# Kernel tuning notes

Hardware: AMD Instinct MI355X
Metric: run time of the kernel (lower is better)

The kernel has to match this reference:

```python
import jax, jax.numpy as jnp
import numpy as np

N_VOX = 100000   # active voxels
K = 27           # 3^3 kernel offsets
M = 60000        # matched (in, out) pairs per offset
CIN = 64
COUT = 64
BN_EPS = 1e-5


def setup_inputs() -> dict:
    key = jax.random.key(0)
    ks = jax.random.split(key, 6)
    feats = jax.random.normal(ks[0], (N_VOX, CIN), dtype=jnp.float32)
    W = jax.random.normal(ks[1], (K, CIN, COUT), dtype=jnp.float32) * 0.05
    gamma = jnp.ones((COUT,), dtype=jnp.float32)
    beta = jnp.zeros((COUT,), dtype=jnp.float32)
    running_mean = jax.random.normal(ks[2], (COUT,), dtype=jnp.float32) * 0.1
    running_var = jax.random.uniform(ks[3], (COUT,), dtype=jnp.float32, minval=0.5, maxval=1.5)
    in_idx = jax.random.randint(ks[4], (K, M), 0, N_VOX, dtype=jnp.int32)
    out_idx = jax.random.randint(ks[5], (K, M), 0, N_VOX, dtype=jnp.int32)
    return {
        "feats": feats, "W": W, "gamma": gamma, "beta": beta,
        "running_mean": running_mean, "running_var": running_var,
        "in_idx": in_idx, "out_idx": out_idx,
    }


def reference(feats, W, gamma, beta, running_mean, running_var, in_idx, out_idx):
    # Sparse conv as gather-GEMM-scatter over the hash-map kernel map.
    gathered = feats[in_idx]                              # [K, M, Cin]
    contrib = jnp.einsum('kmc,kcd->kmd', gathered, W)     # [K, M, Cout]
    out = jax.ops.segment_sum(
        contrib.reshape(-1, W.shape[-1]),                 # [K*M, Cout]
        out_idx.reshape(-1),
        num_segments=feats.shape[0],
    )                                                     # [N, Cout]
    # BatchNorm (inference, running stats) + ReLU
    inv = jax.lax.rsqrt(running_var + BN_EPS)
    y = (out - running_mean) * (inv * gamma) + beta
    return jnp.maximum(y, 0.0)
```

## Files before the change

### kernel.cpp

```cpp
#include <hip/hip_runtime.h>

#define N_VOX 100000
#define K_OFF 27
#define M_PAIR 60000
#define NPAIR (K_OFF * M_PAIR)
#define CIN 64
#define COUT 64
#define BN_EPS 1e-5f

#define VB_SHIFT 8
#define VB (1 << VB_SHIFT)
#define NB ((N_VOX + VB - 1) / VB)
#define BCAP 5120
#define PPT 16
#define PA_PAIRS (256 * PPT)
#define PA_GRID ((NPAIR + PA_PAIRS - 1) / PA_PAIRS)

#define TILES_PER_WAVE 10
#define WAVES_PER_K (M_PAIR / 16 / TILES_PER_WAVE)
#define CONV_BLOCKS_X ((WAVES_PER_K + 3) / 4)

typedef __attribute__((ext_vector_type(8))) short bf16x8;
typedef __attribute__((ext_vector_type(8))) unsigned short u16x8;
typedef __attribute__((ext_vector_type(4))) unsigned int u32x4;
typedef __attribute__((ext_vector_type(2))) int i32x2;
typedef __attribute__((ext_vector_type(4))) float f32x4;

__device__ __forceinline__ unsigned short f32_to_bf16(float f) {
    unsigned int u = __float_as_uint(f);
    u += 0x7FFFu + ((u >> 16) & 1u);
    return (unsigned short)(u >> 16);
}
__device__ __forceinline__ float bf16_lo(unsigned int u) {
    return __uint_as_float(u << 16);
}
__device__ __forceinline__ float bf16_hi(unsigned int u) {
    return __uint_as_float(u & 0xffff0000u);
}

__global__ __launch_bounds__(256) void prep_kernel(
    const float* __restrict__ feats, unsigned short* __restrict__ fb,
    const float* __restrict__ W, unsigned short* __restrict__ Wt,
    const float* __restrict__ gamma, const float* __restrict__ beta,
    const float* __restrict__ rmean, const float* __restrict__ rvar,
    float* __restrict__ bnscale, float* __restrict__ bnshift,
    int* __restrict__ bucketCount)
{
    const int gid = blockIdx.x * 256 + threadIdx.x;
    const int nt = gridDim.x * 256;
    for (int e4i = gid; e4i < (N_VOX * CIN) / 4; e4i += nt) {
        const int e4 = e4i * 4;
        const float4 v = *(const float4*)(feats + e4);
        ushort4 b;
        b.x = f32_to_bf16(v.x);
        b.y = f32_to_bf16(v.y);
        b.z = f32_to_bf16(v.z);
        b.w = f32_to_bf16(v.w);
        *(ushort4*)(fb + e4) = b;
    }
    for (int e = gid; e < K_OFF * CIN * COUT; e += nt) {
        const int k = e / (CIN * COUT);
        const int r = e % (CIN * COUT);
        Wt[k * CIN * COUT + (r % COUT) * CIN + (r / COUT)] = f32_to_bf16(W[e]);
    }
    if (gid < COUT) {
        const float inv = rsqrtf(rvar[gid] + BN_EPS);
        const float sc = inv * gamma[gid];
        bnscale[gid] = sc;
        bnshift[gid] = beta[gid] - rmean[gid] * sc;
    }
    if (gid < NB) bucketCount[gid] = 0;
}

__global__ __launch_bounds__(256) void conv_bucket_kernel(
    const unsigned short* __restrict__ fb, const unsigned short* __restrict__ Wt,
    const int* __restrict__ in_idx, const int* __restrict__ oix,
    unsigned int* __restrict__ recs, int* __restrict__ bucketCount,
    unsigned short* __restrict__ contrib)
{
    __shared__ alignas(16) unsigned short lds[4][16 * 72];
    __shared__ int lhist[NB];
    __shared__ int gbase[NB];
    const int t = threadIdx.x;
    const int k = blockIdx.y;
    const int fid = k * CONV_BLOCKS_X + blockIdx.x;

    if (fid < PA_GRID) {
        for (int i = t; i < NB; i += 256) lhist[i] = 0;
        __syncthreads();
        const int base = fid * PA_PAIRS;
        int lp[PPT];
#pragma unroll
        for (int i = 0; i < PPT; ++i) {
            const int e = base + i * 256 + t;
            lp[i] = (e < NPAIR) ? atomicAdd(&lhist[oix[e] >> VB_SHIFT], 1) : 0;
        }
        __syncthreads();
        for (int i = t; i < NB; i += 256) {
            const int c = lhist[i];
            gbase[i] = c ? atomicAdd(&bucketCount[i], c) : 0;
        }
        __syncthreads();
#pragma unroll
        for (int i = 0; i < PPT; ++i) {
            const int e = base + i * 256 + t;
            if (e < NPAIR) {
                const int v = oix[e];
                const int b = v >> VB_SHIFT;
                const int idx = gbase[b] + lp[i];
                if (idx < BCAP)
                    recs[(size_t)b * BCAP + idx] =
                        ((unsigned int)e << VB_SHIFT) | (unsigned int)(v & (VB - 1));
            }
        }
    }

    const int lane = threadIdx.x & 63;
    const int wid = threadIdx.x >> 6;
    const int w = blockIdx.x * 4 + wid;
    if (w >= WAVES_PER_K) return;
    const int col = lane & 15;
    const int quad = lane >> 4;
    unsigned short* L = lds[wid];

    bf16x8 Bf[4][2];
    const short* Wk = (const short*)(Wt + k * CIN * COUT);
#pragma unroll
    for (int tt = 0; tt < 4; ++tt) {
        const short* p = Wk + (tt * 16 + col) * CIN + quad * 8;
        Bf[tt][0] = *(const bf16x8*)(p);
        Bf[tt][1] = *(const bf16x8*)(p + 32);
    }

    int m0 = k * M_PAIR + (w * TILES_PER_WAVE) * 16;
    {
        const int rin = in_idx[m0 + col];
        const short* fp = (const short*)fb + (size_t)rin * CIN + quad * 8;
        bf16x8 A0 = *(const bf16x8*)(fp);
        bf16x8 A1 = *(const bf16x8*)(fp + 32);

        for (int it = 0; it < TILES_PER_WAVE; ++it) {
            bf16x8 nA0 = A0, nA1 = A1;
            if (it + 1 < TILES_PER_WAVE) {
                const int rn = in_idx[m0 + 16 + col];
                const short* fn = (const short*)fb + (size_t)rn * CIN + quad * 8;
                nA0 = *(const bf16x8*)(fn);
                nA1 = *(const bf16x8*)(fn + 32);
            }

            f32x4 acc[4];
#pragma unroll
            for (int tt = 0; tt < 4; ++tt) {
                f32x4 z = {0.f, 0.f, 0.f, 0.f};
                acc[tt] = __builtin_amdgcn_mfma_f32_16x16x32_bf16(A0, Bf[tt][0], z, 0, 0, 0);
                acc[tt] = __builtin_amdgcn_mfma_f32_16x16x32_bf16(A1, Bf[tt][1], acc[tt], 0, 0, 0);
            }
#pragma unroll
            for (int r = 0; r < 4; ++r) {
                const int row = quad * 4 + r;
#pragma unroll
                for (int tt = 0; tt < 4; ++tt)
                    L[row * 72 + tt * 16 + col] = f32_to_bf16(acc[tt][r]);
            }
#pragma unroll
            for (int itr = 0; itr < 2; ++itr) {
                const int row = itr * 8 + (lane >> 3);
                const int chunk = lane & 7;
                const u16x8 v = *(const u16x8*)(L + row * 72 + chunk * 8);
                *(u16x8*)(contrib + (size_t)(m0 + row) * 64 + chunk * 8) = v;
            }
            A0 = nA0;
            A1 = nA1;
            m0 += 16;
        }
    }
}

__global__ __launch_bounds__(512) void perm_seg_kernel(
    const unsigned int* __restrict__ recs, const int* __restrict__ bucketCount,
    int* __restrict__ perm, i32x2* __restrict__ segcnt)
{
    __shared__ int scan[512];
    __shared__ int hist[VB];
    __shared__ int gb_sh, bc_sh;
    const int b = blockIdx.x;
    const int t = threadIdx.x;
    int c = 0;
    if (t < NB) {
        c = bucketCount[t];
        if (c > BCAP) c = BCAP;
    }
    scan[t] = c;
    __syncthreads();
    for (int o = 1; o < 512; o <<= 1) {
        int x = (t >= o) ? scan[t - o] : 0;
        __syncthreads();
        scan[t] += x;
        __syncthreads();
    }
    if (t == b) {
        gb_sh = scan[t] - c;
        bc_sh = c;
    }
    if (t < VB) hist[t] = 0;
    __syncthreads();
    const int bc = bc_sh;
    const int gbase = gb_sh;
    const unsigned int* r = recs + (size_t)b * BCAP;
    for (int i = t; i < bc; i += 512)
        atomicAdd(&hist[r[i] & (VB - 1)], 1);
    __syncthreads();
    int hc = 0;
    if (t < VB) {
        hc = hist[t];
        scan[t] = hc;
    }
    __syncthreads();
    for (int o = 1; o < VB; o <<= 1) {
        int x = (t < VB && t >= o) ? scan[t - o] : 0;
        __syncthreads();
        if (t < VB) scan[t] += x;
        __syncthreads();
    }
    if (t < VB) {
        const int excl = scan[t] - hc;
        const int v = b * VB + t;
        if (v < N_VOX) {
            i32x2 sc2;
            sc2.x = gbase + excl;
            sc2.y = hc;
            segcnt[v] = sc2;
        }
        hist[t] = excl;
    }
    __syncthreads();
    for (int i = t; i < bc; i += 512) {
        const unsigned int rec = r[i];
        const int lp = atomicAdd(&hist[rec & (VB - 1)], 1);
        perm[gbase + lp] = (int)(rec >> VB_SHIFT);
    }
}

__global__ __launch_bounds__(256) void gather_bn_kernel(
    const unsigned short* __restrict__ contrib, const int* __restrict__ perm,
    const i32x2* __restrict__ segcnt,
    const float* __restrict__ bnscale, const float* __restrict__ bnshift,
    float* __restrict__ out)
{
    const int v = blockIdx.x * 4 + (threadIdx.x >> 6);
    if (v >= N_VOX) return;
    const int lane = threadIdx.x & 63;
    const int rg = lane >> 3;
    const int cg = lane & 7;
    const i32x2 sc = segcnt[v];
    const int s = sc.x;
    const int n = sc.y;

    float a0 = 0.f, a1 = 0.f, a2 = 0.f, a3 = 0.f;
    float a4 = 0.f, a5 = 0.f, a6 = 0.f, a7 = 0.f;
    float b0 = 0.f, b1 = 0.f, b2 = 0.f, b3 = 0.f;
    float b4 = 0.f, b5 = 0.f, b6 = 0.f, b7 = 0.f;
    int j = rg;
    for (; j + 8 < n; j += 16) {
        const int p0 = perm[s + j];
        const int p1 = perm[s + j + 8];
        const u32x4 u = __builtin_nontemporal_load(
            (const u32x4*)(contrib + (size_t)p0 * 64) + cg);
        const u32x4 w = __builtin_nontemporal_load(
            (const u32x4*)(contrib + (size_t)p1 * 64) + cg);
        a0 += bf16_lo(u.x); a1 += bf16_hi(u.x);
        a2 += bf16_lo(u.y); a3 += bf16_hi(u.y);
        a4 += bf16_lo(u.z); a5 += bf16_hi(u.z);
        a6 += bf16_lo(u.w); a7 += bf16_hi(u.w);
        b0 += bf16_lo(w.x); b1 += bf16_hi(w.x);
        b2 += bf16_lo(w.y); b3 += bf16_hi(w.y);
        b4 += bf16_lo(w.z); b5 += bf16_hi(w.z);
        b6 += bf16_lo(w.w); b7 += bf16_hi(w.w);
    }
    for (; j < n; j += 8) {
        const int p0 = perm[s + j];
        const u32x4 u = __builtin_nontemporal_load(
            (const u32x4*)(contrib + (size_t)p0 * 64) + cg);
        a0 += bf16_lo(u.x); a1 += bf16_hi(u.x);
        a2 += bf16_lo(u.y); a3 += bf16_hi(u.y);
        a4 += bf16_lo(u.z); a5 += bf16_hi(u.z);
        a6 += bf16_lo(u.w); a7 += bf16_hi(u.w);
    }
    a0 += b0; a1 += b1; a2 += b2; a3 += b3;
    a4 += b4; a5 += b5; a6 += b6; a7 += b7;
    a0 += __shfl_xor(a0, 8, 64); a0 += __shfl_xor(a0, 16, 64); a0 += __shfl_xor(a0, 32, 64);
    a1 += __shfl_xor(a1, 8, 64); a1 += __shfl_xor(a1, 16, 64); a1 += __shfl_xor(a1, 32, 64);
    a2 += __shfl_xor(a2, 8, 64); a2 += __shfl_xor(a2, 16, 64); a2 += __shfl_xor(a2, 32, 64);
    a3 += __shfl_xor(a3, 8, 64); a3 += __shfl_xor(a3, 16, 64); a3 += __shfl_xor(a3, 32, 64);
    a4 += __shfl_xor(a4, 8, 64); a4 += __shfl_xor(a4, 16, 64); a4 += __shfl_xor(a4, 32, 64);
    a5 += __shfl_xor(a5, 8, 64); a5 += __shfl_xor(a5, 16, 64); a5 += __shfl_xor(a5, 32, 64);
    a6 += __shfl_xor(a6, 8, 64); a6 += __shfl_xor(a6, 16, 64); a6 += __shfl_xor(a6, 32, 64);
    a7 += __shfl_xor(a7, 8, 64); a7 += __shfl_xor(a7, 16, 64); a7 += __shfl_xor(a7, 32, 64);
    if (rg == 0) {
        const int ch = cg * 8;
        float4 r0, r1;
        r0.x = fmaxf(fmaf(a0, bnscale[ch + 0], bnshift[ch + 0]), 0.f);
        r0.y = fmaxf(fmaf(a1, bnscale[ch + 1], bnshift[ch + 1]), 0.f);
        r0.z = fmaxf(fmaf(a2, bnscale[ch + 2], bnshift[ch + 2]), 0.f);
        r0.w = fmaxf(fmaf(a3, bnscale[ch + 3], bnshift[ch + 3]), 0.f);
        r1.x = fmaxf(fmaf(a4, bnscale[ch + 4], bnshift[ch + 4]), 0.f);
        r1.y = fmaxf(fmaf(a5, bnscale[ch + 5], bnshift[ch + 5]), 0.f);
        r1.z = fmaxf(fmaf(a6, bnscale[ch + 6], bnshift[ch + 6]), 0.f);
        r1.w = fmaxf(fmaf(a7, bnscale[ch + 7], bnshift[ch + 7]), 0.f);
        *(float4*)(out + (size_t)v * 64 + ch) = r0;
        *(float4*)(out + (size_t)v * 64 + ch + 4) = r1;
    }
}

__global__ __launch_bounds__(256) void prep_small_kernel(
    const float* __restrict__ feats, unsigned short* __restrict__ fb,
    float* __restrict__ out, const float* __restrict__ W,
    unsigned short* __restrict__ Wt)
{
    const int e = blockIdx.x * blockDim.x + threadIdx.x;
    if (e < (N_VOX * CIN) / 4) {
        const int e4 = e * 4;
        const float4 v = *(const float4*)(feats + e4);
        ushort4 b;
        b.x = f32_to_bf16(v.x);
        b.y = f32_to_bf16(v.y);
        b.z = f32_to_bf16(v.z);
        b.w = f32_to_bf16(v.w);
        *(ushort4*)(fb + e4) = b;
        *(float4*)(out + e4) = make_float4(0.f, 0.f, 0.f, 0.f);
    }
    if (e < K_OFF * CIN * COUT) {
        const int k = e / (CIN * COUT);
        const int r = e % (CIN * COUT);
        Wt[k * CIN * COUT + (r % COUT) * CIN + (r / COUT)] = f32_to_bf16(W[e]);
    }
}

__global__ __launch_bounds__(256) void conv_atomic_kernel(
    const unsigned short* __restrict__ fb, const unsigned short* __restrict__ Wt,
    const int* __restrict__ in_idx, const int* __restrict__ out_idx,
    float* __restrict__ out)
{
    const int k = blockIdx.y;
    const int lane = threadIdx.x & 63;
    const int wave = blockIdx.x * 4 + (threadIdx.x >> 6);
    const int col = lane & 15;
    const int quad = lane >> 4;
    bf16x8 Bf[4][2];
    const short* Wk = (const short*)(Wt + k * CIN * COUT);
#pragma unroll
    for (int t = 0; t < 4; ++t) {
        const short* p = Wk + (t * 16 + col) * CIN + quad * 8;
        Bf[t][0] = *(const bf16x8*)(p);
        Bf[t][1] = *(const bf16x8*)(p + 32);
    }
    const int base = k * M_PAIR;
    for (int tile = wave; tile < M_PAIR / 16; tile += 128) {
        const int m0 = base + tile * 16;
        const int rin = in_idx[m0 + col];
        const short* fp = (const short*)fb + (size_t)rin * CIN + quad * 8;
        const bf16x8 A0 = *(const bf16x8*)(fp);
        const bf16x8 A1 = *(const bf16x8*)(fp + 32);
        f32x4 acc[4];
#pragma unroll
        for (int t = 0; t < 4; ++t) {
            f32x4 z = {0.f, 0.f, 0.f, 0.f};
            acc[t] = __builtin_amdgcn_mfma_f32_16x16x32_bf16(A0, Bf[t][0], z, 0, 0, 0);
            acc[t] = __builtin_amdgcn_mfma_f32_16x16x32_bf16(A1, Bf[t][1], acc[t], 0, 0, 0);
        }
        int vo[4];
#pragma unroll
        for (int r = 0; r < 4; ++r) vo[r] = out_idx[m0 + quad * 4 + r];
#pragma unroll
        for (int r = 0; r < 4; ++r) {
            float* op = out + (size_t)vo[r] * COUT + col;
#pragma unroll
            for (int t = 0; t < 4; ++t) atomicAdd(op + t * 16, acc[t][r]);
        }
    }
}

__global__ __launch_bounds__(256) void bn_relu_kernel(
    float* __restrict__ out,
    const float* __restrict__ gamma, const float* __restrict__ beta,
    const float* __restrict__ mean, const float* __restrict__ var)
{
    const int e = blockIdx.x * blockDim.x + threadIdx.x;
    if (e >= N_VOX * COUT) return;
    const int c = e & (COUT - 1);
    const float inv = rsqrtf(var[c] + BN_EPS);
    const float y = (out[e] - mean[c]) * (inv * gamma[c]) + beta[c];
    out[e] = fmaxf(y, 0.f);
}

extern "C" void kernel_launch(void* const* d_in, const int* in_sizes, int n_in,
                              void* d_out, int out_size, void* d_ws, size_t ws_size,
                              hipStream_t stream) {
    const float* feats = (const float*)d_in[0];
    const float* W     = (const float*)d_in[1];
    const float* gamma = (const float*)d_in[2];
    const float* beta  = (const float*)d_in[3];
    const float* rmean = (const float*)d_in[4];
    const float* rvar  = (const float*)d_in[5];
    const int* in_idx  = (const int*)d_in[6];
    const int* out_idx = (const int*)d_in[7];
    float* out = (float*)d_out;

    char* ws = (char*)d_ws;
    size_t off = 0;
    auto alloc = [&](size_t bytes) {
        size_t p = off;
        off = (off + bytes + 255) & ~(size_t)255;
        return p;
    };
    const size_t o_fb   = alloc((size_t)N_VOX * CIN * 2);
    const size_t o_wt   = alloc((size_t)K_OFF * CIN * COUT * 2);
    const size_t o_bc   = alloc((size_t)NB * 4);
    const size_t o_recs = alloc((size_t)NB * BCAP * 4);
    const size_t o_sc   = alloc((size_t)N_VOX * 8);
    const size_t o_bn   = alloc((size_t)2 * COUT * 4);
    const size_t o_perm = alloc((size_t)NPAIR * 4);
    const size_t o_ctr  = alloc((size_t)NPAIR * COUT * 2);
    const bool big = (ws_size >= off);

    unsigned short* fb  = (unsigned short*)(ws + o_fb);
    unsigned short* Wt  = (unsigned short*)(ws + o_wt);
    int* bucketCount    = (int*)(ws + o_bc);
    unsigned int* recs  = (unsigned int*)(ws + o_recs);
    i32x2* segcnt       = (i32x2*)(ws + o_sc);
    float* bnscale      = (float*)(ws + o_bn);
    float* bnshift      = bnscale + COUT;
    int* perm           = (int*)(ws + o_perm);
    unsigned short* ctr = (unsigned short*)(ws + o_ctr);

    if (big) {
        prep_kernel<<<2048, 256, 0, stream>>>(
            feats, fb, W, Wt, gamma, beta, rmean, rvar,
            bnscale, bnshift, bucketCount);
        conv_bucket_kernel<<<dim3(CONV_BLOCKS_X, K_OFF), 256, 0, stream>>>(
            fb, Wt, in_idx, out_idx, recs, bucketCount, ctr);
        perm_seg_kernel<<<NB, 512, 0, stream>>>(recs, bucketCount, perm, segcnt);
        gather_bn_kernel<<<(N_VOX + 3) / 4, 256, 0, stream>>>(
            ctr, perm, segcnt, bnscale, bnshift, out);
    } else {
        const int ptot = (N_VOX * CIN) / 4;
        prep_small_kernel<<<(ptot + 255) / 256, 256, 0, stream>>>(feats, fb, out, W, Wt);
        conv_atomic_kernel<<<dim3(32, K_OFF), 256, 0, stream>>>(fb, Wt, in_idx, out_idx, out);
        const int total_e = N_VOX * COUT;
        bn_relu_kernel<<<(total_e + 255) / 256, 256, 0, stream>>>(out, gamma, beta, rmean, rvar);
    }
}
```

Before: 228.0 us.

## Fuse per-bucket permutation build into gather+BN kernel using shared-memory local perm

Merges the per-bucket counting-sort kernel and the gather/BN/ReLU kernel. Each block now takes a quarter of a voxel bucket, builds its segment offsets and pair permutation in shared memory, then gathers the bf16 contributions and applies BN+ReLU. This drops the global perm and segcnt arrays and one launch. In exchange every block rescans the whole bucket's records, four times redundantly across the quarters, and uses only NB*4 blocks. A quarter holding more than QCAP pairs would be truncated.

```diff
diff --git a/kernel.cpp b/kernel.cpp
--- a/kernel.cpp
+++ b/kernel.cpp
@@ -16,6 +16,10 @@
 #define PA_PAIRS (256 * PPT)
 #define PA_GRID ((NPAIR + PA_PAIRS - 1) / PA_PAIRS)
 
+#define QSPLIT 4
+#define QVOX (VB / QSPLIT)
+#define QCAP 1280
+
 #define TILES_PER_WAVE 10
 #define WAVES_PER_K (M_PAIR / 16 / TILES_PER_WAVE)
 #define CONV_BLOCKS_X ((WAVES_PER_K + 3) / 4)
@@ -23,7 +27,6 @@
 typedef __attribute__((ext_vector_type(8))) short bf16x8;
 typedef __attribute__((ext_vector_type(8))) unsigned short u16x8;
 typedef __attribute__((ext_vector_type(4))) unsigned int u32x4;
-typedef __attribute__((ext_vector_type(2))) int i32x2;
 typedef __attribute__((ext_vector_type(4))) float f32x4;
 
 __device__ __forceinline__ unsigned short f32_to_bf16(float f) {
@@ -176,139 +179,117 @@
     }
 }
 
-__global__ __launch_bounds__(512) void perm_seg_kernel(
+__global__ __launch_bounds__(256) void gather_bn_kernel(
     const unsigned int* __restrict__ recs, const int* __restrict__ bucketCount,
-    int* __restrict__ perm, i32x2* __restrict__ segcnt)
-{
-    __shared__ int scan[512];
-    __shared__ int hist[VB];
-    __shared__ int gb_sh, bc_sh;
-    const int b = blockIdx.x;
+    const unsigned short* __restrict__ contrib,
+    const float* __restrict__ bnscale, const float* __restrict__ bnshift,
+    float* __restrict__ out)
+{
+    __shared__ int hist[QVOX];
+    __shared__ int scan_[QVOX];
+    __shared__ int cursor[QVOX];
+    __shared__ int lperm[QCAP];
+    __shared__ float s_sc[COUT], s_sh[COUT];
+    const int blk = blockIdx.x;
+    const int b = blk >> 2;
+    const int q = blk & 3;
     const int t = threadIdx.x;
-    int c = 0;
-    if (t < NB) {
-        c = bucketCount[t];
-        if (c > BCAP) c = BCAP;
-    }
-    scan[t] = c;
+    if (t < QVOX) hist[t] = 0;
+    if (t < COUT) { s_sc[t] = bnscale[t]; s_sh[t] = bnshift[t]; }
     __syncthreads();
-    for (int o = 1; o < 512; o <<= 1) {
-        int x = (t >= o) ? scan[t - o] : 0;
-        __syncthreads();
-        scan[t] += x;
-        __syncthreads();
-    }
-    if (t == b) {
-        gb_sh = scan[t] - c;
-        bc_sh = c;
-    }
-    if (t < VB) hist[t] = 0;
-    __syncthreads();
-    const int bc = bc_sh;
-    const int gbase = gb_sh;
+    int bc = bucketCount[b];
+    if (bc > BCAP) bc = BCAP;
     const unsigned int* r = recs + (size_t)b * BCAP;
-    for (int i = t; i < bc; i += 512)
-        atomicAdd(&hist[r[i] & (VB - 1)], 1);
+    for (int i = t; i < bc; i += 256) {
+        const int vl = r[i] & (VB - 1);
+        if ((vl >> 6) == q) atomicAdd(&hist[vl & (QVOX - 1)], 1);
+    }
     __syncthreads();
     int hc = 0;
-    if (t < VB) {
-        hc = hist[t];
-        scan[t] = hc;
-    }
+    if (t < QVOX) { hc = hist[t]; scan_[t] = hc; }
     __syncthreads();
-    for (int o = 1; o < VB; o <<= 1) {
-        int x = (t < VB && t >= o) ? scan[t - o] : 0;
+    for (int o = 1; o < QVOX; o <<= 1) {
+        int x = (t < QVOX && t >= o) ? scan_[t - o] : 0;
         __syncthreads();
-        if (t < VB) scan[t] += x;
+        if (t < QVOX) scan_[t] += x;
         __syncthreads();
     }
-    if (t < VB) {
-        const int excl = scan[t] - hc;
-        const int v = b * VB + t;
-        if (v < N_VOX) {
-            i32x2 sc2;
-            sc2.x = gbase + excl;
-            sc2.y = hc;
-            segcnt[v] = sc2;
-        }
-        hist[t] = excl;
-    }
+    if (t < QVOX) cursor[t] = scan_[t] - hc;
     __syncthreads();
-    for (int i = t; i < bc; i += 512) {
+    for (int i = t; i < bc; i += 256) {
         const unsigned int rec = r[i];
-        const int lp = atomicAdd(&hist[rec & (VB - 1)], 1);
-        perm[gbase + lp] = (int)(rec >> VB_SHIFT);
-    }
-}
-
-__global__ __launch_bounds__(256) void gather_bn_kernel(
-    const unsigned short* __restrict__ contrib, const int* __restrict__ perm,
-    const i32x2* __restrict__ segcnt,
-    const float* __restrict__ bnscale, const float* __restrict__ bnshift,
-    float* __restrict__ out)
-{
-    const int v = blockIdx.x * 4 + (threadIdx.x >> 6);
-    if (v >= N_VOX) return;
-    const int lane = threadIdx.x & 63;
+        const int vl = rec & (VB - 1);
+        if ((vl >> 6) == q) {
+            const int lp = atomicAdd(&cursor[vl & (QVOX - 1)], 1);
+            if (lp < QCAP) lperm[lp] = (int)(rec >> VB_SHIFT);
+        }
+    }
+    __syncthreads();
+    const int wid = t >> 6;
+    const int lane = t & 63;
     const int rg = lane >> 3;
     const int cg = lane & 7;
-    const i32x2 sc = segcnt[v];
-    const int s = sc.x;
-    const int n = sc.y;
-
-    float a0 = 0.f, a1 = 0.f, a2 = 0.f, a3 = 0.f;
-    float a4 = 0.f, a5 = 0.f, a6 = 0.f, a7 = 0.f;
-    float b0 = 0.f, b1 = 0.f, b2 = 0.f, b3 = 0.f;
-    float b4 = 0.f, b5 = 0.f, b6 = 0.f, b7 = 0.f;
-    int j = rg;
-    for (; j + 8 < n; j += 16) {
-        const int p0 = perm[s + j];
-        const int p1 = perm[s + j + 8];
-        const u32x4 u = __builtin_nontemporal_load(
-            (const u32x4*)(contrib + (size_t)p0 * 64) + cg);
-        const u32x4 w = __builtin_nontemporal_load(
-            (const u32x4*)(contrib + (size_t)p1 * 64) + cg);
-        a0 += bf16_lo(u.x); a1 += bf16_hi(u.x);
-        a2 += bf16_lo(u.y); a3 += bf16_hi(u.y);
-        a4 += bf16_lo(u.z); a5 += bf16_hi(u.z);
-        a6 += bf16_lo(u.w); a7 += bf16_hi(u.w);
-        b0 += bf16_lo(w.x); b1 += bf16_hi(w.x);
-        b2 += bf16_lo(w.y); b3 += bf16_hi(w.y);
-        b4 += bf16_lo(w.z); b5 += bf16_hi(w.z);
-        b6 += bf16_lo(w.w); b7 += bf16_hi(w.w);
-    }
-    for (; j < n; j += 8) {
-        const int p0 = perm[s + j];
-        const u32x4 u = __builtin_nontemporal_load(
-            (const u32x4*)(contrib + (size_t)p0 * 64) + cg);
-        a0 += bf16_lo(u.x); a1 += bf16_hi(u.x);
-        a2 += bf16_lo(u.y); a3 += bf16_hi(u.y);
-        a4 += bf16_lo(u.z); a5 += bf16_hi(u.z);
-        a6 += bf16_lo(u.w); a7 += bf16_hi(u.w);
-    }
-    a0 += b0; a1 += b1; a2 += b2; a3 += b3;
-    a4 += b4; a5 += b5; a6 += b6; a7 += b7;
-    a0 += __shfl_xor(a0, 8, 64); a0 += __shfl_xor(a0, 16, 64); a0 += __shfl_xor(a0, 32, 64);
-    a1 += __shfl_xor(a1, 8, 64); a1 += __shfl_xor(a1, 16, 64); a1 += __shfl_xor(a1, 32, 64);
-    a2 += __shfl_xor(a2, 8, 64); a2 += __shfl_xor(a2, 16, 64); a2 += __shfl_xor(a2, 32, 64);
-    a3 += __shfl_xor(a3, 8, 64); a3 += __shfl_xor(a3, 16, 64); a3 += __shfl_xor(a3, 32, 64);
-    a4 += __shfl_xor(a4, 8, 64); a4 += __shfl_xor(a4, 16, 64); a4 += __shfl_xor(a4, 32, 64);
-    a5 += __shfl_xor(a5, 8, 64); a5 += __shfl_xor(a5, 16, 64); a5 += __shfl_xor(a5, 32, 64);
-    a6 += __shfl_xor(a6, 8, 64); a6 += __shfl_xor(a6, 16, 64); a6 += __shfl_xor(a6, 32, 64);
-    a7 += __shfl_xor(a7, 8, 64); a7 += __shfl_xor(a7, 16, 64); a7 += __shfl_xor(a7, 32, 64);
-    if (rg == 0) {
-        const int ch = cg * 8;
-        float4 r0, r1;
-        r0.x = fmaxf(fmaf(a0, bnscale[ch + 0], bnshift[ch + 0]), 0.f);
-        r0.y = fmaxf(fmaf(a1, bnscale[ch + 1], bnshift[ch + 1]), 0.f);
-        r0.z = fmaxf(fmaf(a2, bnscale[ch + 2], bnshift[ch + 2]), 0.f);
-        r0.w = fmaxf(fmaf(a3, bnscale[ch + 3], bnshift[ch + 3]), 0.f);
-        r1.x = fmaxf(fmaf(a4, bnscale[ch + 4], bnshift[ch + 4]), 0.f);
-        r1.y = fmaxf(fmaf(a5, bnscale[ch + 5], bnshift[ch + 5]), 0.f);
-        r1.z = fmaxf(fmaf(a6, bnscale[ch + 6], bnshift[ch + 6]), 0.f);
-        r1.w = fmaxf(fmaf(a7, bnscale[ch + 7], bnshift[ch + 7]), 0.f);
-        *(float4*)(out + (size_t)v * 64 + ch) = r0;
-        *(float4*)(out + (size_t)v * 64 + ch + 4) = r1;
+    for (int vi = wid; vi < QVOX; vi += 4) {
+        const int v = b * VB + q * QVOX + vi;
+        if (v >= N_VOX) continue;
+        int n = hist[vi];
+        const int s = scan_[vi] - n;
+        if (s + n > QCAP) n = (s < QCAP) ? QCAP - s : 0;
+
+        float a0 = 0.f, a1 = 0.f, a2 = 0.f, a3 = 0.f;
+        float a4 = 0.f, a5 = 0.f, a6 = 0.f, a7 = 0.f;
+        float b0 = 0.f, b1 = 0.f, b2 = 0.f, b3 = 0.f;
+        float b4 = 0.f, b5 = 0.f, b6 = 0.f, b7 = 0.f;
+        int j = rg;
+        for (; j + 8 < n; j += 16) {
+            const int p0 = lperm[s + j];
+            const int p1 = lperm[s + j + 8];
+            const u32x4 u = __builtin_nontemporal_load(
+                (const u32x4*)(contrib + (size_t)p0 * 64) + cg);
+            const u32x4 w = __builtin_nontemporal_load(
+                (const u32x4*)(contrib + (size_t)p1 * 64) + cg);
+            a0 += bf16_lo(u.x); a1 += bf16_hi(u.x);
+            a2 += bf16_lo(u.y); a3 += bf16_hi(u.y);
+            a4 += bf16_lo(u.z); a5 += bf16_hi(u.z);
+            a6 += bf16_lo(u.w); a7 += bf16_hi(u.w);
+            b0 += bf16_lo(w.x); b1 += bf16_hi(w.x);
+            b2 += bf16_lo(w.y); b3 += bf16_hi(w.y);
+            b4 += bf16_lo(w.z); b5 += bf16_hi(w.z);
+            b6 += bf16_lo(w.w); b7 += bf16_hi(w.w);
+        }
+        for (; j < n; j += 8) {
+            const int p0 = lperm[s + j];
+            const u32x4 u = __builtin_nontemporal_load(
+                (const u32x4*)(contrib + (size_t)p0 * 64) + cg);
+            a0 += bf16_lo(u.x); a1 += bf16_hi(u.x);
+            a2 += bf16_lo(u.y); a3 += bf16_hi(u.y);
+            a4 += bf16_lo(u.z); a5 += bf16_hi(u.z);
+            a6 += bf16_lo(u.w); a7 += bf16_hi(u.w);
+        }
+        a0 += b0; a1 += b1; a2 += b2; a3 += b3;
+        a4 += b4; a5 += b5; a6 += b6; a7 += b7;
+        a0 += __shfl_xor(a0, 8, 64); a0 += __shfl_xor(a0, 16, 64); a0 += __shfl_xor(a0, 32, 64);
+        a1 += __shfl_xor(a1, 8, 64); a1 += __shfl_xor(a1, 16, 64); a1 += __shfl_xor(a1, 32, 64);
+        a2 += __shfl_xor(a2, 8, 64); a2 += __shfl_xor(a2, 16, 64); a2 += __shfl_xor(a2, 32, 64);
+        a3 += __shfl_xor(a3, 8, 64); a3 += __shfl_xor(a3, 16, 64); a3 += __shfl_xor(a3, 32, 64);
+        a4 += __shfl_xor(a4, 8, 64); a4 += __shfl_xor(a4, 16, 64); a4 += __shfl_xor(a4, 32, 64);
+        a5 += __shfl_xor(a5, 8, 64); a5 += __shfl_xor(a5, 16, 64); a5 += __shfl_xor(a5, 32, 64);
+        a6 += __shfl_xor(a6, 8, 64); a6 += __shfl_xor(a6, 16, 64); a6 += __shfl_xor(a6, 32, 64);
+        a7 += __shfl_xor(a7, 8, 64); a7 += __shfl_xor(a7, 16, 64); a7 += __shfl_xor(a7, 32, 64);
+        if (rg == 0) {
+            const int ch = cg * 8;
+            float4 r0, r1;
+            r0.x = fmaxf(fmaf(a0, s_sc[ch + 0], s_sh[ch + 0]), 0.f);
+            r0.y = fmaxf(fmaf(a1, s_sc[ch + 1], s_sh[ch + 1]), 0.f);
+            r0.z = fmaxf(fmaf(a2, s_sc[ch + 2], s_sh[ch + 2]), 0.f);
+            r0.w = fmaxf(fmaf(a3, s_sc[ch + 3], s_sh[ch + 3]), 0.f);
+            r1.x = fmaxf(fmaf(a4, s_sc[ch + 4], s_sh[ch + 4]), 0.f);
+            r1.y = fmaxf(fmaf(a5, s_sc[ch + 5], s_sh[ch + 5]), 0.f);
+            r1.z = fmaxf(fmaf(a6, s_sc[ch + 6], s_sh[ch + 6]), 0.f);
+            r1.w = fmaxf(fmaf(a7, s_sc[ch + 7], s_sh[ch + 7]), 0.f);
+            *(float4*)(out + (size_t)v * 64 + ch) = r0;
+            *(float4*)(out + (size_t)v * 64 + ch + 4) = r1;
+        }
     }
 }
 
@@ -417,9 +398,7 @@
     const size_t o_wt   = alloc((size_t)K_OFF * CIN * COUT * 2);
     const size_t o_bc   = alloc((size_t)NB * 4);
     const size_t o_recs = alloc((size_t)NB * BCAP * 4);
-    const size_t o_sc   = alloc((size_t)N_VOX * 8);
     const size_t o_bn   = alloc((size_t)2 * COUT * 4);
-    const size_t o_perm = alloc((size_t)NPAIR * 4);
     const size_t o_ctr  = alloc((size_t)NPAIR * COUT * 2);
     const bool big = (ws_size >= off);
 
@@ -427,10 +406,8 @@
     unsigned short* Wt  = (unsigned short*)(ws + o_wt);
     int* bucketCount    = (int*)(ws + o_bc);
     unsigned int* recs  = (unsigned int*)(ws + o_recs);
-    i32x2* segcnt       = (i32x2*)(ws + o_sc);
     float* bnscale      = (float*)(ws + o_bn);
     float* bnshift      = bnscale + COUT;
-    int* perm           = (int*)(ws + o_perm);
     unsigned short* ctr = (unsigned short*)(ws + o_ctr);
 
     if (big) {
@@ -439,9 +416,8 @@
             bnscale, bnshift, bucketCount);
         conv_bucket_kernel<<<dim3(CONV_BLOCKS_X, K_OFF), 256, 0, stream>>>(
             fb, Wt, in_idx, out_idx, recs, bucketCount, ctr);
-        perm_seg_kernel<<<NB, 512, 0, stream>>>(recs, bucketCount, perm, segcnt);
-        gather_bn_kernel<<<(N_VOX + 3) / 4, 256, 0, stream>>>(
-            ctr, perm, segcnt, bnscale, bnshift, out);
+        gather_bn_kernel<<<NB * QSPLIT, 256, 0, stream>>>(
+            recs, bucketCount, ctr, bnscale, bnshift, out);
     } else {
         const int ptot = (N_VOX * CIN) / 4;
         prep_small_kernel<<<(ptot + 255) / 256, 256, 0, stream>>>(feats, fb, out, W, Wt);
```

Measured after the change: 226.4 us, median of 2. About the same (-0.7%).
